# Optimization experiments

Measured on AMD Instinct MI355X. Metric: run time of the kernel, lower is better.

Reference implementation:

```python
import jax, jax.numpy as jnp
import numpy as np

HARMONICS = 5


def _harmonic_basis(x):
    k = jnp.arange(1, HARMONICS + 1, dtype=x.dtype)            # [H]
    kx = x[..., None] * k                                       # [B, D, H]
    sc = jnp.stack([jnp.sin(kx), jnp.cos(kx)], axis=-1)         # [B, D, H, 2]
    sc = sc.reshape(*x.shape, 2 * HARMONICS)                    # interleaved sin/cos
    ones = jnp.ones((*x.shape, 1), dtype=x.dtype)
    return jnp.concatenate([ones, sc], axis=-1)                 # [B, D, 2H+1]


def setup_inputs() -> dict:
    key = jax.random.key(0)
    k1, k2, k3 = jax.random.split(key, 3)
    B, D, F, H = 16384, 256, 11, 256
    x = jax.random.normal(k1, (B, D), dtype=jnp.float32)
    W = jax.random.normal(k2, (D, F, H), dtype=jnp.float32) * (1.0 / np.sqrt(F))
    b = jax.random.normal(k3, (D, H), dtype=jnp.float32) * 0.01
    return {"x": x, "W": W, "b": b}


def reference(x, W, b) -> jnp.ndarray:
    # basis expansion per feature, batched small GEMM, summed over features
    basis = _harmonic_basis(x)                                  # [B, D, F]
    out = jnp.einsum('bdf,dfh->bh', basis, W)                   # sum over features fused
    out = out + jnp.sum(b, axis=0)                              # sum of per-feature biases
    return out
```

## Files before the change

kernel.cpp:

```cpp
#include <hip/hip_runtime.h>
#include <hip/hip_bf16.h>


#define HOUT 256
#define DDIM 256
#define NKT  80

typedef __bf16 bf16x8 __attribute__((ext_vector_type(8)));
typedef float floatx4 __attribute__((ext_vector_type(4)));

__device__ __forceinline__ unsigned short f2bf(float f) {
    unsigned int u = __float_as_uint(f);
    return (unsigned short)((u + 0x7FFFu + ((u >> 16) & 1u)) >> 16);
}

__device__ __forceinline__ unsigned int pkbf(float a, float b) {
    __hip_bfloat162 r = __float22bfloat162_rn(make_float2(a, b));
    return *reinterpret_cast<unsigned int*>(&r);
}

__device__ __forceinline__ float harm(int hs, float s1, float c1, float c2) {
    switch (hs) {
    case 0: return s1;
    case 1: return c1;
    case 2: return (s1 + s1) * c1;
    case 3: return c2;
    case 4: return __builtin_fmaf(c2 + c2, s1, s1);
    case 5: return __builtin_fmaf(c2 + c2, c1, -c1);
    case 6: return (c2 + c2) * ((s1 + s1) * c1);
    case 7: return __builtin_fmaf(c2 + c2, c2, -1.f);
    case 8: { const float s3 = __builtin_fmaf(c2 + c2, s1, s1);
              return __builtin_fmaf(c2 + c2, s3, -s1); }
    case 9: { const float c3 = __builtin_fmaf(c2 + c2, c1, -c1);
              return __builtin_fmaf(c2 + c2, c3, -c1); }
    }
    return 0.f;
}

__global__ void prep_kernel(const float* __restrict__ W, const float* __restrict__ bias,
                            unsigned short* __restrict__ Wfrag, float* __restrict__ c_part) {
    const int bid = blockIdx.x;
    const int t = threadIdx.x;
    if (bid < NKT) {
        const int kt = bid;
        const int dtile = kt / 10;
        const int f = kt - dtile * 10 + 1;
        const float* wsrc = W + ((size_t)(dtile * 32) * 11 + f) * 256 + t;
        union { unsigned short s[32]; int4 v[4]; } buf;
#pragma unroll
        for (int dd = 0; dd < 32; ++dd)
            buf.s[dd] = f2bf(wsrc[(size_t)dd * 11 * 256]);
        int4* dst = (int4*)(Wfrag + ((size_t)kt * 256 + t) * 32);
#pragma unroll
        for (int v = 0; v < 4; ++v) dst[v] = buf.v[v];
    } else {
        const int p = bid - NKT;
        float acc = 0.f;
#pragma unroll
        for (int dd = 0; dd < 32; ++dd) {
            const int d = p * 32 + dd;
            acc += W[(size_t)(d * 11) * 256 + t] + bias[(size_t)d * 256 + t];
        }
        c_part[p * 256 + t] = acc;
    }
}

__global__ __launch_bounds__(256, 2)
void kan_gemm(const float* __restrict__ x, const unsigned short* __restrict__ Wfrag,
              const float* __restrict__ c_part, float* __restrict__ out) {
    const int t = threadIdx.x;
    const int lane = t & 63;
    const int wave = t >> 6;
    const int l15 = lane & 15;
    const int koff = lane >> 4;

    const int m0 = blockIdx.x * 128 + wave * 32;
    const int n0 = blockIdx.y * 64;

    const unsigned short* bptr = Wfrag + (size_t)(n0 + l15) * 32 + koff * 8;

    const float* xbase = x + (size_t)(m0 + l15) * DDIM + koff * 8;

    floatx4 acc[2][4];
#pragma unroll
    for (int it = 0; it < 2; ++it)
#pragma unroll
        for (int jt = 0; jt < 4; ++jt)
            acc[it][jt] = (floatx4){0.f, 0.f, 0.f, 0.f};

    float4 xq[4];
#pragma unroll
    for (int it = 0; it < 2; ++it) {
        xq[2 * it]     = *(const float4*)(xbase + it * 16 * DDIM);
        xq[2 * it + 1] = *(const float4*)(xbase + it * 16 * DDIM + 4);
    }

    bf16x8 bc[4], bn[4];
#pragma unroll
    for (int jt = 0; jt < 4; ++jt)
        bc[jt] = *(const bf16x8*)(bptr + jt * 512);

    float s1[2][8], c1[2][8], c2[2][8];

    for (int dtile = 0; dtile < 8; ++dtile) {
#pragma unroll
        for (int it = 0; it < 2; ++it) {
            const float xs[8] = {xq[2 * it].x, xq[2 * it].y, xq[2 * it].z, xq[2 * it].w,
                                 xq[2 * it + 1].x, xq[2 * it + 1].y, xq[2 * it + 1].z, xq[2 * it + 1].w};
#pragma unroll
            for (int jj = 0; jj < 8; ++jj) {
                float s, c;
                __sincosf(xs[jj], &s, &c);
                s1[it][jj] = s;
                c1[it][jj] = c;
                c2[it][jj] = __builtin_fmaf(c + c, c, -1.f);
            }
        }

        if (dtile < 7) {
            const float* xn = xbase + (dtile + 1) * 32;
#pragma unroll
            for (int it = 0; it < 2; ++it) {
                xq[2 * it]     = *(const float4*)(xn + it * 16 * DDIM);
                xq[2 * it + 1] = *(const float4*)(xn + it * 16 * DDIM + 4);
            }
        }

        const unsigned short* bkt = bptr + (size_t)dtile * 10 * 8192;

#pragma unroll
        for (int hs = 0; hs < 10; ++hs) {
#pragma unroll
            for (int jt = 0; jt < 4; ++jt)
                bn[jt] = *(const bf16x8*)(bkt + (size_t)(hs + 1) * 8192 + jt * 512);

            bf16x8 af[2];
#pragma unroll
            for (int it = 0; it < 2; ++it) {
                union { unsigned int u[4]; bf16x8 v; } a;
#pragma unroll
                for (int p = 0; p < 4; ++p) {
                    const float va = harm(hs, s1[it][2 * p], c1[it][2 * p], c2[it][2 * p]);
                    const float vb = harm(hs, s1[it][2 * p + 1], c1[it][2 * p + 1], c2[it][2 * p + 1]);
                    a.u[p] = pkbf(va, vb);
                }
                af[it] = a.v;
            }

#pragma unroll
            for (int it = 0; it < 2; ++it)
#pragma unroll
                for (int jt = 0; jt < 4; ++jt)
                    acc[it][jt] = __builtin_amdgcn_mfma_f32_16x16x32_bf16(af[it], bc[jt], acc[it][jt], 0, 0, 0);

#pragma unroll
            for (int jt = 0; jt < 4; ++jt)
                bc[jt] = bn[jt];
        }
    }

    float cj[4];
#pragma unroll
    for (int jt = 0; jt < 4; ++jt) {
        const int col = n0 + jt * 16 + l15;
        float s = 0.f;
#pragma unroll
        for (int p = 0; p < 8; ++p) s += c_part[p * 256 + col];
        cj[jt] = s;
    }
#pragma unroll
    for (int it = 0; it < 2; ++it) {
        const int row0 = m0 + it * 16 + koff * 4;
#pragma unroll
        for (int jt = 0; jt < 4; ++jt) {
            const int col = n0 + jt * 16 + l15;
#pragma unroll
            for (int r = 0; r < 4; ++r)
                out[(size_t)(row0 + r) * HOUT + col] = acc[it][jt][r] + cj[jt];
        }
    }
}

extern "C" void kernel_launch(void* const* d_in, const int* in_sizes, int n_in,
                              void* d_out, int out_size, void* d_ws, size_t ws_size,
                              hipStream_t stream) {
    const float* x = (const float*)d_in[0];
    const float* W = (const float*)d_in[1];
    const float* b = (const float*)d_in[2];
    float* out = (float*)d_out;

    unsigned short* Wfrag = (unsigned short*)d_ws;
    float* c_part = (float*)((char*)d_ws + (size_t)NKT * 256 * 32 * 2);

    prep_kernel<<<NKT + 8, 256, 0, stream>>>(W, b, Wfrag, c_part);
    kan_gemm<<<dim3(128, 4), 256, 0, stream>>>(x, Wfrag, c_part, out);
}
```

Baseline: 120.6 us.

## Software-pipeline harmonic A-fragment generation against MFMAs in two halves

Splits the ten harmonic k-slices into two groups of five (sin-like and cos-like orders) and reorders the packed weights to match via a feature map. A-fragments for one half are generated while MFMAs consume the other, and sin/cos of the next d-tile plus the x loads are issued during the second half, so VALU work overlaps matrix math. It also replaces the bf16 conversion intrinsic with a manual round-and-perm pack and uses separate __sinf/__cosf calls. The cost is higher register pressure from holding ten A-fragments plus double-buffered B fragments, which could cause spills at two blocks per CU.

```diff
diff --git a/kernel.cpp b/kernel.cpp
--- a/kernel.cpp
+++ b/kernel.cpp
@@ -14,28 +14,36 @@
     return (unsigned short)((u + 0x7FFFu + ((u >> 16) & 1u)) >> 16);
 }
 
-__device__ __forceinline__ unsigned int pkbf(float a, float b) {
-    __hip_bfloat162 r = __float22bfloat162_rn(make_float2(a, b));
-    return *reinterpret_cast<unsigned int*>(&r);
-}
-
-__device__ __forceinline__ float harm(int hs, float s1, float c1, float c2) {
-    switch (hs) {
-    case 0: return s1;
-    case 1: return c1;
-    case 2: return (s1 + s1) * c1;
-    case 3: return c2;
-    case 4: return __builtin_fmaf(c2 + c2, s1, s1);
-    case 5: return __builtin_fmaf(c2 + c2, c1, -c1);
-    case 6: return (c2 + c2) * ((s1 + s1) * c1);
-    case 7: return __builtin_fmaf(c2 + c2, c2, -1.f);
-    case 8: { const float s3 = __builtin_fmaf(c2 + c2, s1, s1);
-              return __builtin_fmaf(c2 + c2, s3, -s1); }
-    case 9: { const float c3 = __builtin_fmaf(c2 + c2, c1, -c1);
-              return __builtin_fmaf(c2 + c2, c3, -c1); }
-    }
-    return 0.f;
-}
+__device__ __forceinline__ unsigned int bfpair(float a, float b) {
+    unsigned int ua = __float_as_uint(a), ub = __float_as_uint(b);
+    ua += 0x7FFFu + ((ua >> 16) & 1u);
+    ub += 0x7FFFu + ((ub >> 16) & 1u);
+    return __builtin_amdgcn_perm(ub, ua, 0x07060302u);
+}
+
+__device__ __forceinline__ float hval(int half, int q, float s1, float c1) {
+    if (half == 0) {
+        if (q == 0) return s1;
+        if (q == 1) return c1;
+        const float c2 = __builtin_fmaf(c1 + c1, c1, -1.f);
+        const float tc = c2 + c2;
+        if (q == 2) return __builtin_fmaf(tc, s1, s1);
+        if (q == 3) return __builtin_fmaf(tc, c1, -c1);
+        const float s3 = __builtin_fmaf(tc, s1, s1);
+        return __builtin_fmaf(tc, s3, -s1);
+    } else {
+        const float c2 = __builtin_fmaf(c1 + c1, c1, -1.f);
+        if (q == 1) return c2;
+        if (q == 0) return (s1 + s1) * c1;
+        const float tc = c2 + c2;
+        if (q == 2) return tc * ((s1 + s1) * c1);
+        if (q == 3) return __builtin_fmaf(tc, c2, -1.f);
+        const float c3 = __builtin_fmaf(tc, c1, -c1);
+        return __builtin_fmaf(tc, c3, -c1);
+    }
+}
+
+__device__ __constant__ int FMAP[10] = {1, 2, 5, 6, 9, 3, 4, 7, 8, 10};
 
 __global__ void prep_kernel(const float* __restrict__ W, const float* __restrict__ bias,
                             unsigned short* __restrict__ Wfrag, float* __restrict__ c_part) {
@@ -44,7 +52,7 @@
     if (bid < NKT) {
         const int kt = bid;
         const int dtile = kt / 10;
-        const int f = kt - dtile * 10 + 1;
+        const int f = FMAP[kt - dtile * 10];
         const float* wsrc = W + ((size_t)(dtile * 32) * 11 + f) * 256 + t;
         union { unsigned short s[32]; int4 v[4]; } buf;
 #pragma unroll
@@ -65,12 +73,36 @@
     }
 }
 
+__device__ __forceinline__ void scchunk(int it, const float4 xq[4],
+                                        float s1[2][8], float c1[2][8]) {
+    const float4 xa = xq[2 * it], xb = xq[2 * it + 1];
+    const float xs[8] = {xa.x, xa.y, xa.z, xa.w, xb.x, xb.y, xb.z, xb.w};
+#pragma unroll
+    for (int jj = 0; jj < 8; ++jj) {
+        s1[it][jj] = __sinf(xs[jj]);
+        c1[it][jj] = __cosf(xs[jj]);
+    }
+}
+
+__device__ __forceinline__ void genchunk(bf16x8 dst[2][5], int half, int q,
+                                         const float s1[2][8], const float c1[2][8]) {
+#pragma unroll
+    for (int it = 0; it < 2; ++it) {
+        union { unsigned int u[4]; bf16x8 v; } r;
+#pragma unroll
+        for (int p = 0; p < 4; ++p)
+            r.u[p] = bfpair(hval(half, q, s1[it][2 * p], c1[it][2 * p]),
+                            hval(half, q, s1[it][2 * p + 1], c1[it][2 * p + 1]));
+        dst[it][q] = r.v;
+    }
+}
+
 __global__ __launch_bounds__(256, 2)
 void kan_gemm(const float* __restrict__ x, const unsigned short* __restrict__ Wfrag,
               const float* __restrict__ c_part, float* __restrict__ out) {
-    const int t = threadIdx.x;
-    const int lane = t & 63;
-    const int wave = t >> 6;
+    const int tid = threadIdx.x;
+    const int lane = tid & 63;
+    const int wave = tid >> 6;
     const int l15 = lane & 15;
     const int koff = lane >> 4;
 
@@ -78,7 +110,6 @@
     const int n0 = blockIdx.y * 64;
 
     const unsigned short* bptr = Wfrag + (size_t)(n0 + l15) * 32 + koff * 8;
-
     const float* xbase = x + (size_t)(m0 + l15) * DDIM + koff * 8;
 
     floatx4 acc[2][4];
@@ -94,68 +125,73 @@
         xq[2 * it]     = *(const float4*)(xbase + it * 16 * DDIM);
         xq[2 * it + 1] = *(const float4*)(xbase + it * 16 * DDIM + 4);
     }
-
-    bf16x8 bc[4], bn[4];
-#pragma unroll
-    for (int jt = 0; jt < 4; ++jt)
-        bc[jt] = *(const bf16x8*)(bptr + jt * 512);
-
-    float s1[2][8], c1[2][8], c2[2][8];
-
-    for (int dtile = 0; dtile < 8; ++dtile) {
-#pragma unroll
-        for (int it = 0; it < 2; ++it) {
-            const float xs[8] = {xq[2 * it].x, xq[2 * it].y, xq[2 * it].z, xq[2 * it].w,
-                                 xq[2 * it + 1].x, xq[2 * it + 1].y, xq[2 * it + 1].z, xq[2 * it + 1].w};
-#pragma unroll
-            for (int jj = 0; jj < 8; ++jj) {
-                float s, c;
-                __sincosf(xs[jj], &s, &c);
-                s1[it][jj] = s;
-                c1[it][jj] = c;
-                c2[it][jj] = __builtin_fmaf(c + c, c, -1.f);
+    bf16x8 bb[2][4];
+#pragma unroll
+    for (int jt = 0; jt < 4; ++jt) bb[0][jt] = *(const bf16x8*)(bptr + jt * 512);
+#pragma unroll
+    for (int jt = 0; jt < 4; ++jt) bb[1][jt] = *(const bf16x8*)(bptr + 8192 + jt * 512);
+
+    float s1[2][8], c1[2][8];
+    scchunk(0, xq, s1, c1);
+    scchunk(1, xq, s1, c1);
+
+    bf16x8 afa[2][5], afb[2][5];
+#pragma unroll
+    for (int q = 0; q < 5; ++q) genchunk(afa, 0, q, s1, c1);
+
+#pragma unroll
+    for (int it = 0; it < 2; ++it) {
+        xq[2 * it]     = *(const float4*)(xbase + 32 + it * 16 * DDIM);
+        xq[2 * it + 1] = *(const float4*)(xbase + 32 + it * 16 * DDIM + 4);
+    }
+
+#pragma unroll 1
+    for (int t = 0; t < 8; ++t) {
+        const unsigned short* bk = bptr + (size_t)(t * 10) * 8192;
+
+#pragma unroll
+        for (int q = 0; q < 5; ++q) {
+#pragma unroll
+            for (int it = 0; it < 2; ++it)
+#pragma unroll
+                for (int jt = 0; jt < 4; ++jt)
+                    acc[it][jt] = __builtin_amdgcn_mfma_f32_16x16x32_bf16(
+                        afa[it][q], bb[q & 1][jt], acc[it][jt], 0, 0, 0);
+#pragma unroll
+            for (int jt = 0; jt < 4; ++jt)
+                bb[q & 1][jt] = *(const bf16x8*)(bk + (size_t)(q + 2) * 8192 + jt * 512);
+            genchunk(afb, 1, q, s1, c1);
+        }
+
+#pragma unroll
+        for (int q = 0; q < 5; ++q) {
+#pragma unroll
+            for (int it = 0; it < 2; ++it)
+#pragma unroll
+                for (int jt = 0; jt < 4; ++jt)
+                    acc[it][jt] = __builtin_amdgcn_mfma_f32_16x16x32_bf16(
+                        afb[it][q], bb[(q + 1) & 1][jt], acc[it][jt], 0, 0, 0);
+            if (q < 3 || t < 7) {
+#pragma unroll
+                for (int jt = 0; jt < 4; ++jt)
+                    bb[(q + 1) & 1][jt] = *(const bf16x8*)(bk + (size_t)(q + 7) * 8192 + jt * 512);
             }
-        }
-
-        if (dtile < 7) {
-            const float* xn = xbase + (dtile + 1) * 32;
-#pragma unroll
-            for (int it = 0; it < 2; ++it) {
-                xq[2 * it]     = *(const float4*)(xn + it * 16 * DDIM);
-                xq[2 * it + 1] = *(const float4*)(xn + it * 16 * DDIM + 4);
+            if (t < 7) {
+                if (q == 0) scchunk(0, xq, s1, c1);
+                if (q == 1) {
+                    scchunk(1, xq, s1, c1);
+                    const int tn = (t + 2 < 8) ? (t + 2) : 7;
+                    const float* xn = xbase + tn * 32;
+#pragma unroll
+                    for (int it = 0; it < 2; ++it) {
+                        xq[2 * it]     = *(const float4*)(xn + it * 16 * DDIM);
+                        xq[2 * it + 1] = *(const float4*)(xn + it * 16 * DDIM + 4);
+                    }
+                }
+                if (q == 2) { genchunk(afa, 0, 0, s1, c1); genchunk(afa, 0, 1, s1, c1); }
+                if (q == 3) { genchunk(afa, 0, 2, s1, c1); genchunk(afa, 0, 3, s1, c1); }
+                if (q == 4) { genchunk(afa, 0, 4, s1, c1); }
             }
-        }
-
-        const unsigned short* bkt = bptr + (size_t)dtile * 10 * 8192;
-
-#pragma unroll
-        for (int hs = 0; hs < 10; ++hs) {
-#pragma unroll
-            for (int jt = 0; jt < 4; ++jt)
-                bn[jt] = *(const bf16x8*)(bkt + (size_t)(hs + 1) * 8192 + jt * 512);
-
-            bf16x8 af[2];
-#pragma unroll
-            for (int it = 0; it < 2; ++it) {
-                union { unsigned int u[4]; bf16x8 v; } a;
-#pragma unroll
-                for (int p = 0; p < 4; ++p) {
-                    const float va = harm(hs, s1[it][2 * p], c1[it][2 * p], c2[it][2 * p]);
-                    const float vb = harm(hs, s1[it][2 * p + 1], c1[it][2 * p + 1], c2[it][2 * p + 1]);
-                    a.u[p] = pkbf(va, vb);
-                }
-                af[it] = a.v;
-            }
-
-#pragma unroll
-            for (int it = 0; it < 2; ++it)
-#pragma unroll
-                for (int jt = 0; jt < 4; ++jt)
-                    acc[it][jt] = __builtin_amdgcn_mfma_f32_16x16x32_bf16(af[it], bc[jt], acc[it][jt], 0, 0, 0);
-
-#pragma unroll
-            for (int jt = 0; jt < 4; ++jt)
-                bc[jt] = bn[jt];
         }
     }
 
```

New measurement: 123.0 us. No clear change (+2.0%).

## Share harmonic basis through LDS and split K across blocks with atomics

Applied to the files above, without the earlier changes.

Each block now computes the sin/cos basis for 64 rows once and stores it as bf16 in double-buffered shared memory. All four waves then reuse it across the full 256 output columns, where before every column block recomputed the basis. The K dimension is split in two across blockIdx.y, so partial sums are combined with float atomic adds into an output zeroed by a memset. This removes redundant transcendental work at the cost of LDS traffic, extra barriers, atomic write traffic and an added memset launch.

```diff
diff --git a/kernel.cpp b/kernel.cpp
--- a/kernel.cpp
+++ b/kernel.cpp
@@ -14,9 +14,11 @@
     return (unsigned short)((u + 0x7FFFu + ((u >> 16) & 1u)) >> 16);
 }
 
-__device__ __forceinline__ unsigned int pkbf(float a, float b) {
-    __hip_bfloat162 r = __float22bfloat162_rn(make_float2(a, b));
-    return *reinterpret_cast<unsigned int*>(&r);
+__device__ __forceinline__ unsigned int bfpair(float a, float b) {
+    unsigned int ua = __float_as_uint(a), ub = __float_as_uint(b);
+    ua += 0x7FFFu + ((ua >> 16) & 1u);
+    ub += 0x7FFFu + ((ub >> 16) & 1u);
+    return __builtin_amdgcn_perm(ub, ua, 0x07060302u);
 }
 
 __device__ __forceinline__ float harm(int hs, float s1, float c1, float c2) {
@@ -68,115 +70,114 @@
 __global__ __launch_bounds__(256, 2)
 void kan_gemm(const float* __restrict__ x, const unsigned short* __restrict__ Wfrag,
               const float* __restrict__ c_part, float* __restrict__ out) {
-    const int t = threadIdx.x;
-    const int lane = t & 63;
-    const int wave = t >> 6;
+    __shared__ unsigned short As[2][10 * 4 * 512];
+
+    const int tid = threadIdx.x;
+    const int lane = tid & 63;
+    const int wave = tid >> 6;
     const int l15 = lane & 15;
     const int koff = lane >> 4;
 
-    const int m0 = blockIdx.x * 128 + wave * 32;
-    const int n0 = blockIdx.y * 64;
+    const int m0 = blockIdx.x * 64;
+    const int khalf = blockIdx.y;
+    const int t0 = khalf * 4;
+    const int kt0 = khalf * 40;
 
-    const unsigned short* bptr = Wfrag + (size_t)(n0 + l15) * 32 + koff * 8;
+    const int r = tid & 63;
+    const int o = tid >> 6;
+    const float* xg = x + (size_t)(m0 + r) * DDIM + o * 8;
+    const int gbase = (r >> 4) * 512 + ((r & 15) + 16 * o) * 8;
 
-    const float* xbase = x + (size_t)(m0 + l15) * DDIM + koff * 8;
+    const unsigned short* bptr = Wfrag + (size_t)(wave * 64 + l15) * 32 + koff * 8;
 
-    floatx4 acc[2][4];
+    floatx4 acc[4][4];
 #pragma unroll
-    for (int it = 0; it < 2; ++it)
+    for (int it = 0; it < 4; ++it)
 #pragma unroll
         for (int jt = 0; jt < 4; ++jt)
             acc[it][jt] = (floatx4){0.f, 0.f, 0.f, 0.f};
 
-    float4 xq[4];
-#pragma unroll
-    for (int it = 0; it < 2; ++it) {
-        xq[2 * it]     = *(const float4*)(xbase + it * 16 * DDIM);
-        xq[2 * it + 1] = *(const float4*)(xbase + it * 16 * DDIM + 4);
-    }
-
-    bf16x8 bc[4], bn[4];
+    bf16x8 bb[2][4];
 #pragma unroll
     for (int jt = 0; jt < 4; ++jt)
-        bc[jt] = *(const bf16x8*)(bptr + jt * 512);
+        bb[0][jt] = *(const bf16x8*)(bptr + (size_t)kt0 * 8192 + jt * 512);
+#pragma unroll
+    for (int jt = 0; jt < 4; ++jt)
+        bb[1][jt] = *(const bf16x8*)(bptr + (size_t)(kt0 + 1) * 8192 + jt * 512);
 
-    float s1[2][8], c1[2][8], c2[2][8];
+    auto gen = [&](int dt, int buf) {
+        const float4 xa = *(const float4*)(xg + dt * 32);
+        const float4 xb = *(const float4*)(xg + dt * 32 + 4);
+        const float xs[8] = {xa.x, xa.y, xa.z, xa.w, xb.x, xb.y, xb.z, xb.w};
+        float s1[8], c1[8], c2[8];
+#pragma unroll
+        for (int jj = 0; jj < 8; ++jj) {
+            s1[jj] = __sinf(xs[jj]);
+            c1[jj] = __cosf(xs[jj]);
+            c2[jj] = __builtin_fmaf(c1[jj] + c1[jj], c1[jj], -1.f);
+        }
+        unsigned short* dst = &As[buf][gbase];
+#pragma unroll
+        for (int hs = 0; hs < 10; ++hs) {
+            union { unsigned int u[4]; int4 q; } v;
+#pragma unroll
+            for (int p = 0; p < 4; ++p)
+                v.u[p] = bfpair(harm(hs, s1[2 * p], c1[2 * p], c2[2 * p]),
+                                harm(hs, s1[2 * p + 1], c1[2 * p + 1], c2[2 * p + 1]));
+            *(int4*)(dst + hs * 2048) = v.q;
+        }
+    };
 
-    for (int dtile = 0; dtile < 8; ++dtile) {
-#pragma unroll
-        for (int it = 0; it < 2; ++it) {
-            const float xs[8] = {xq[2 * it].x, xq[2 * it].y, xq[2 * it].z, xq[2 * it].w,
-                                 xq[2 * it + 1].x, xq[2 * it + 1].y, xq[2 * it + 1].z, xq[2 * it + 1].w};
-#pragma unroll
-            for (int jj = 0; jj < 8; ++jj) {
-                float s, c;
-                __sincosf(xs[jj], &s, &c);
-                s1[it][jj] = s;
-                c1[it][jj] = c;
-                c2[it][jj] = __builtin_fmaf(c + c, c, -1.f);
-            }
-        }
+    gen(t0, 0);
+    __syncthreads();
 
-        if (dtile < 7) {
-            const float* xn = xbase + (dtile + 1) * 32;
-#pragma unroll
-            for (int it = 0; it < 2; ++it) {
-                xq[2 * it]     = *(const float4*)(xn + it * 16 * DDIM);
-                xq[2 * it + 1] = *(const float4*)(xn + it * 16 * DDIM + 4);
-            }
-        }
+#pragma unroll 1
+    for (int td = 0; td < 4; ++td) {
+        if (td < 3) gen(t0 + td + 1, (td + 1) & 1);
 
-        const unsigned short* bkt = bptr + (size_t)dtile * 10 * 8192;
+        const unsigned short* bk = bptr + (size_t)(kt0 + td * 10) * 8192;
+        const unsigned short* abuf = As[td & 1];
 
 #pragma unroll
         for (int hs = 0; hs < 10; ++hs) {
+            bf16x8 af[4];
+#pragma unroll
+            for (int it = 0; it < 4; ++it)
+                af[it] = *(const bf16x8*)(abuf + (hs * 4 + it) * 512 + lane * 8);
+#pragma unroll
+            for (int it = 0; it < 4; ++it)
+#pragma unroll
+                for (int jt = 0; jt < 4; ++jt)
+                    acc[it][jt] = __builtin_amdgcn_mfma_f32_16x16x32_bf16(
+                        af[it], bb[hs & 1][jt], acc[it][jt], 0, 0, 0);
 #pragma unroll
             for (int jt = 0; jt < 4; ++jt)
-                bn[jt] = *(const bf16x8*)(bkt + (size_t)(hs + 1) * 8192 + jt * 512);
+                bb[hs & 1][jt] = *(const bf16x8*)(bk + (size_t)(hs + 2) * 8192 + jt * 512);
+        }
+        __syncthreads();
+    }
 
-            bf16x8 af[2];
+    float cj[4] = {0.f, 0.f, 0.f, 0.f};
+    if (khalf == 0) {
 #pragma unroll
-            for (int it = 0; it < 2; ++it) {
-                union { unsigned int u[4]; bf16x8 v; } a;
+        for (int jt = 0; jt < 4; ++jt) {
+            const int col = wave * 64 + jt * 16 + l15;
+            float s = 0.f;
 #pragma unroll
-                for (int p = 0; p < 4; ++p) {
-                    const float va = harm(hs, s1[it][2 * p], c1[it][2 * p], c2[it][2 * p]);
-                    const float vb = harm(hs, s1[it][2 * p + 1], c1[it][2 * p + 1], c2[it][2 * p + 1]);
-                    a.u[p] = pkbf(va, vb);
-                }
-                af[it] = a.v;
-            }
-
-#pragma unroll
-            for (int it = 0; it < 2; ++it)
-#pragma unroll
-                for (int jt = 0; jt < 4; ++jt)
-                    acc[it][jt] = __builtin_amdgcn_mfma_f32_16x16x32_bf16(af[it], bc[jt], acc[it][jt], 0, 0, 0);
-
-#pragma unroll
-            for (int jt = 0; jt < 4; ++jt)
-                bc[jt] = bn[jt];
+            for (int p = 0; p < 8; ++p) s += c_part[p * 256 + col];
+            cj[jt] = s;
         }
     }
-
-    float cj[4];
 #pragma unroll
-    for (int jt = 0; jt < 4; ++jt) {
-        const int col = n0 + jt * 16 + l15;
-        float s = 0.f;
-#pragma unroll
-        for (int p = 0; p < 8; ++p) s += c_part[p * 256 + col];
-        cj[jt] = s;
-    }
-#pragma unroll
-    for (int it = 0; it < 2; ++it) {
+    for (int it = 0; it < 4; ++it) {
         const int row0 = m0 + it * 16 + koff * 4;
 #pragma unroll
         for (int jt = 0; jt < 4; ++jt) {
-            const int col = n0 + jt * 16 + l15;
+            const int col = wave * 64 + jt * 16 + l15;
 #pragma unroll
-            for (int r = 0; r < 4; ++r)
-                out[(size_t)(row0 + r) * HOUT + col] = acc[it][jt][r] + cj[jt];
+            for (int rr = 0; rr < 4; ++rr)
+                unsafeAtomicAdd(&out[(size_t)(row0 + rr) * HOUT + col],
+                                acc[it][jt][rr] + cj[jt]);
         }
     }
 }
@@ -192,6 +193,7 @@
     unsigned short* Wfrag = (unsigned short*)d_ws;
     float* c_part = (float*)((char*)d_ws + (size_t)NKT * 256 * 32 * 2);
 
+    hipMemsetAsync(out, 0, (size_t)out_size * sizeof(float), stream);
     prep_kernel<<<NKT + 8, 256, 0, stream>>>(W, b, Wfrag, c_part);
-    kan_gemm<<<dim3(128, 4), 256, 0, stream>>>(x, Wfrag, c_part, out);
+    kan_gemm<<<dim3(256, 2), 256, 0, stream>>>(x, Wfrag, c_part, out);
 }
```

Result: no change. 122.0 us (+1.2%).
